# Performance work log

Hardware: AMD Instinct MI355X
Metric: run time of the kernel (lower is better)

Reference implementation:

```python
import jax, jax.numpy as jnp
import numpy as np

B, S, H, D = 16, 1024, 8, 128
HID = 1024
EPS = 1e-5
ALPHA = 1.0 / (D ** 0.5)
SILU_SCALE = 1.0 / S  # silu_scale = 1/max_seq_len


def _layer_norm(x, w, b):
    mu = jnp.mean(x, axis=-1, keepdims=True)
    var = jnp.mean(jnp.square(x - mu), axis=-1, keepdims=True)
    return (x - mu) * jax.lax.rsqrt(var + EPS) * w + b


def setup_inputs() -> dict:
    key = jax.random.key(0)
    ks = jax.random.split(key, 4)
    N = B * S
    return {
        "x": jax.random.normal(ks[0], (N, HID), dtype=jnp.float32),
        "ln_in_w": jnp.ones((HID,), jnp.float32),
        "ln_in_b": jnp.zeros((HID,), jnp.float32),
        "W_uvqk": jax.random.normal(ks[1], (4 * H * D, HID), jnp.float32) * (HID ** -0.5),
        "b_uvqk": jax.random.normal(ks[2], (4 * H * D,), jnp.float32) * 0.1,
        "ln_out_w": jnp.ones((H * D,), jnp.float32),
        "ln_out_b": jnp.zeros((H * D,), jnp.float32),
        "W_proj": jax.random.normal(ks[3], (H * D, HID), jnp.float32) * ((H * D) ** -0.5),
    }


def reference(x, ln_in_w, ln_in_b, W_uvqk, b_uvqk, ln_out_w, ln_out_b, W_proj):
    # x: [N, HID] jagged tokens (rectangular: B seqs of length S)
    normed = _layer_norm(x, ln_in_w, ln_in_b)
    mixed = jax.nn.silu(normed @ W_uvqk.T + b_uvqk)          # [N, 4*H*D]
    u, v, q, k = jnp.split(mixed, 4, axis=-1)
    q = q.reshape(B, S, H, D)
    k = k.reshape(B, S, H, D)
    v = v.reshape(B, S, H, D)
    # HSTU attention: silu(q.k^T * alpha) * silu_scale, causal per sequence
    scores = jnp.einsum("bshd,bthd->bhst", q, k) * ALPHA      # [B,H,S,S]
    w = jax.nn.silu(scores) * SILU_SCALE
    causal = jnp.tril(jnp.ones((S, S), dtype=bool))
    w = jnp.where(causal, w, 0.0)
    attn = jnp.einsum("bhst,bthd->bshd", w, v).reshape(B * S, H * D)
    parallel = u * _layer_norm(attn, ln_out_w, ln_out_b)
    out = parallel @ W_proj + x  # residual
    return out
```

## Files before the change

### kernel.cpp

```cpp
#include <hip/hip_runtime.h>

typedef __bf16 bf16x8 __attribute__((ext_vector_type(8)));
typedef float f32x4 __attribute__((ext_vector_type(4)));
typedef unsigned short u16x4 __attribute__((ext_vector_type(4)));
typedef unsigned short u16x8 __attribute__((ext_vector_type(8)));

#define DEVI __device__ __forceinline__

DEVI unsigned short f2b(float f) {
  union { float f; unsigned u; } v; v.f = f;
  unsigned r = (v.u + 0x7FFFu + ((v.u >> 16) & 1u)) >> 16;
  return (unsigned short)r;
}
DEVI float b2f(unsigned short h) {
  union { unsigned u; float f; } v; v.u = ((unsigned)h) << 16;
  return v.f;
}
DEVI float silu_f(float v) { return v / (1.f + __expf(-v)); }

DEVI void gload_lds16(const void* g, void* l) {
  __builtin_amdgcn_global_load_lds(
      (const __attribute__((address_space(1))) unsigned int*)g,
      (__attribute__((address_space(3))) unsigned int*)l, 16, 0, 0);
}

#define ALPHA 0.08838834764831845f
#define SILU_SCALE 0.0009765625f
#define LN_EPS 1e-5f

__global__ __launch_bounds__(256, 4) void cvt_bf16_kernel(
    const float* __restrict__ src, unsigned short* __restrict__ dst, int n4) {
  int i = blockIdx.x * 256 + threadIdx.x;
  int stride = gridDim.x * 256;
  for (; i < n4; i += stride) {
    f32x4 f = ((const f32x4*)src)[i];
    u16x4 o;
    #pragma unroll
    for (int j = 0; j < 4; ++j) o[j] = f2b(f[j]);
    ((u16x4*)dst)[i] = o;
  }
}

__global__ __launch_bounds__(256, 4) void transpose_wp_kernel(
    const float* __restrict__ Wp, unsigned short* __restrict__ WpT) {
  __shared__ unsigned short lT[64 * 68];
  int tid = threadIdx.x;
  int r0 = blockIdx.y * 64, c0 = blockIdx.x * 64;
  #pragma unroll
  for (int p = 0; p < 4; ++p) {
    int r = p * 16 + (tid >> 4);
    int c = (tid & 15) * 4;
    f32x4 f = *(const f32x4*)(Wp + (size_t)(r0 + r) * 1024 + c0 + c);
    #pragma unroll
    for (int i = 0; i < 4; ++i) lT[(c + i) * 68 + r] = f2b(f[i]);
  }
  __syncthreads();
  #pragma unroll
  for (int p = 0; p < 4; ++p) {
    int j = p * 16 + (tid >> 4);
    int i0 = (tid & 15) * 4;
    u16x4 o;
    #pragma unroll
    for (int q = 0; q < 4; ++q) o[q] = lT[j * 68 + i0 + q];
    *(u16x4*)(WpT + (size_t)(c0 + j) * 1024 + r0 + i0) = o;
  }
}

__global__ __launch_bounds__(256, 4) void ln1_kernel(
    const float* __restrict__ x, const float* __restrict__ w,
    const float* __restrict__ bwt, unsigned short* __restrict__ out) {
  __shared__ float red[8];
  int row = blockIdx.x, tid = threadIdx.x;
  f32x4 f = ((const f32x4*)(x + (size_t)row * 1024))[tid];
  float s1 = f[0] + f[1] + f[2] + f[3];
  float s2 = f[0] * f[0] + f[1] * f[1] + f[2] * f[2] + f[3] * f[3];
  #pragma unroll
  for (int off = 32; off > 0; off >>= 1) {
    s1 += __shfl_down(s1, off);
    s2 += __shfl_down(s2, off);
  }
  if ((tid & 63) == 0) { red[(tid >> 6) * 2] = s1; red[(tid >> 6) * 2 + 1] = s2; }
  __syncthreads();
  s1 = red[0] + red[2] + red[4] + red[6];
  s2 = red[1] + red[3] + red[5] + red[7];
  float mu = s1 * (1.f / 1024.f);
  float rstd = rsqrtf(s2 * (1.f / 1024.f) - mu * mu + LN_EPS);
  f32x4 wv = ((const f32x4*)w)[tid];
  f32x4 bv = ((const f32x4*)bwt)[tid];
  u16x4 o;
  #pragma unroll
  for (int i = 0; i < 4; ++i) o[i] = f2b((f[i] - mu) * rstd * wv[i] + bv[i]);
  ((u16x4*)(out + (size_t)row * 1024))[tid] = o;
}

__global__ __launch_bounds__(256, 4) void ln2_kernel(
    const unsigned short* __restrict__ attn, unsigned short* __restrict__ mixed,
    const float* __restrict__ w, const float* __restrict__ bwt) {
  __shared__ float red[8];
  int row = blockIdx.x, tid = threadIdx.x;
  u16x4 av = ((const u16x4*)(attn + (size_t)row * 1024))[tid];
  float f0 = b2f(av[0]), f1 = b2f(av[1]), f2v = b2f(av[2]), f3 = b2f(av[3]);
  float s1 = f0 + f1 + f2v + f3;
  float s2 = f0 * f0 + f1 * f1 + f2v * f2v + f3 * f3;
  #pragma unroll
  for (int off = 32; off > 0; off >>= 1) {
    s1 += __shfl_down(s1, off);
    s2 += __shfl_down(s2, off);
  }
  if ((tid & 63) == 0) { red[(tid >> 6) * 2] = s1; red[(tid >> 6) * 2 + 1] = s2; }
  __syncthreads();
  s1 = red[0] + red[2] + red[4] + red[6];
  s2 = red[1] + red[3] + red[5] + red[7];
  float mu = s1 * (1.f / 1024.f);
  float rstd = rsqrtf(s2 * (1.f / 1024.f) - mu * mu + LN_EPS);
  f32x4 wv = ((const f32x4*)w)[tid];
  f32x4 bv = ((const f32x4*)bwt)[tid];
  u16x4 uv = ((const u16x4*)(mixed + (size_t)row * 4096))[tid];
  float n0 = (f0 - mu) * rstd * wv[0] + bv[0];
  float n1 = (f1 - mu) * rstd * wv[1] + bv[1];
  float n2 = (f2v - mu) * rstd * wv[2] + bv[2];
  float n3 = (f3 - mu) * rstd * wv[3] + bv[3];
  u16x4 o;
  o[0] = f2b(b2f(uv[0]) * n0);
  o[1] = f2b(b2f(uv[1]) * n1);
  o[2] = f2b(b2f(uv[2]) * n2);
  o[3] = f2b(b2f(uv[3]) * n3);
  ((u16x4*)(mixed + (size_t)row * 4096 + 1024))[tid] = o;
}

template <int EPI>
__global__ __launch_bounds__(256, 2) void gemm_bt_kernel(
    const unsigned short* __restrict__ A, int lda,
    const unsigned short* __restrict__ Bt, int ldb,
    unsigned short* __restrict__ Cb, float* __restrict__ Cf, int ldc,
    const float* __restrict__ aux, int K) {
  __shared__ unsigned short lA[128 * 64];
  __shared__ unsigned short lB[128 * 64];
  const int tid = threadIdx.x, wave = tid >> 6, lane = tid & 63;
  const int row0 = blockIdx.x * 128, col0 = blockIdx.y * 128;
  const int wr = wave >> 1, wc = wave & 1;
  const int sr = tid >> 3;
  const int kel = ((tid & 7) ^ (sr & 7)) * 8;
  f32x4 acc[4][4] = {};
  for (int k0 = 0; k0 < K; k0 += 64) {
    #pragma unroll
    for (int is = 0; is < 4; ++is) {
      int r = is * 32 + sr;
      gload_lds16(A + (size_t)(row0 + r) * lda + k0 + kel, lA + is * 2048 + wave * 512);
      gload_lds16(Bt + (size_t)(col0 + r) * ldb + k0 + kel, lB + is * 2048 + wave * 512);
    }
    __syncthreads();
    #pragma unroll
    for (int kk = 0; kk < 2; ++kk) {
      const int cb = (lane >> 4) * 16 + kk * 64;
      bf16x8 af[4], bfr[4];
      #pragma unroll
      for (int i = 0; i < 4; ++i) {
        int ra = wr * 64 + i * 16 + (lane & 15);
        af[i] = *(const bf16x8*)(lA + ra * 64 + ((cb ^ ((ra & 7) << 4)) >> 1));
        int rb = wc * 64 + i * 16 + (lane & 15);
        bfr[i] = *(const bf16x8*)(lB + rb * 64 + ((cb ^ ((rb & 7) << 4)) >> 1));
      }
      #pragma unroll
      for (int i = 0; i < 4; ++i)
        #pragma unroll
        for (int j = 0; j < 4; ++j)
          acc[i][j] = __builtin_amdgcn_mfma_f32_16x16x32_bf16(af[i], bfr[j], acc[i][j], 0, 0, 0);
    }
    __syncthreads();
  }
  const int cr = (lane >> 4) * 4, cc = lane & 15;
  #pragma unroll
  for (int i = 0; i < 4; ++i) {
    int grow0 = row0 + wr * 64 + i * 16 + cr;
    #pragma unroll
    for (int j = 0; j < 4; ++j) {
      int gcol = col0 + wc * 64 + j * 16 + cc;
      if (EPI == 0) {
        float bvv = aux[gcol];
        #pragma unroll
        for (int r = 0; r < 4; ++r)
          Cb[(size_t)(grow0 + r) * ldc + gcol] = f2b(silu_f(acc[i][j][r] + bvv));
      } else {
        #pragma unroll
        for (int r = 0; r < 4; ++r) {
          size_t idx = (size_t)(grow0 + r) * ldc + gcol;
          Cf[idx] = acc[i][j][r] + aux[idx];
        }
      }
    }
  }
}

__global__ __launch_bounds__(256, 4) void vtrans_kernel(
    const unsigned short* __restrict__ mixed, unsigned short* __restrict__ vT) {
  __shared__ unsigned short lT[128 * 64];
  const int tid = threadIdx.x;
  const int s0 = blockIdx.x * 64, h = blockIdx.y, b = blockIdx.z;
  const unsigned short* vp = mixed + (size_t)b * 1024 * 4096 + 1024 + h * 128;
  #pragma unroll
  for (int p = 0; p < 4; ++p) {
    int sl = p * 16 + (tid >> 4);
    int d0 = (tid & 15) * 8;
    u16x8 val = *(const u16x8*)(vp + (size_t)(s0 + sl) * 4096 + d0);
    #pragma unroll
    for (int i = 0; i < 8; ++i) {
      int d = d0 + i;
      lT[d * 64 + ((((sl * 2) ^ ((((d >> 3) & 7)) << 4))) >> 1)] = val[i];
    }
  }
  __syncthreads();
  unsigned short* op = vT + (size_t)(b * 8 + h) * 128 * 1024;
  #pragma unroll
  for (int p = 0; p < 4; ++p) {
    int d = p * 32 + (tid >> 3);
    int sg = (tid & 7) * 8;
    u16x8 o = *(const u16x8*)(lT + d * 64 + ((((sg * 2) ^ ((((d >> 3) & 7)) << 4))) >> 1));
    *(u16x8*)(op + (size_t)d * 1024 + s0 + sg) = o;
  }
}

__global__ __launch_bounds__(256, 2) void attn_kernel(
    const unsigned short* __restrict__ mixed, const unsigned short* __restrict__ vT,
    unsigned short* __restrict__ attnout) {
  __shared__ unsigned short lK[64 * 128];
  __shared__ unsigned short lV[128 * 64];
  __shared__ unsigned short lW[4 * 16 * 64];
  const int tid = threadIdx.x, wave = tid >> 6, lane = tid & 63;
  const int blkq = blockIdx.x, h = blockIdx.y, b = blockIdx.z;
  const int Q0 = blkq * 64;
  const size_t rowbase = (size_t)b * 1024 * 4096;
  const unsigned short* qp = mixed + rowbase + 2048 + h * 128;
  const unsigned short* kp = mixed + rowbase + 3072 + h * 128;
  const unsigned short* vp = vT + (size_t)(b * 8 + h) * 128 * 1024;
  bf16x8 qf[4];
  {
    int qrow = Q0 + wave * 16 + (lane & 15);
    #pragma unroll
    for (int kk = 0; kk < 4; ++kk)
      qf[kk] = *(const bf16x8*)(qp + (size_t)qrow * 4096 + (lane >> 4) * 8 + kk * 32);
  }
  f32x4 oacc[8] = {};
  unsigned short* lWw = lW + wave * 1024;
  for (int t0 = 0; t0 <= Q0; t0 += 64) {
    {
      int rr = tid >> 4, gg = tid & 15;
      #pragma unroll
      for (int is = 0; is < 4; ++is) {
        int row = is * 16 + rr;
        gload_lds16(kp + (size_t)(t0 + row) * 4096 + (size_t)((gg ^ (row & 7)) * 8),
                    lK + is * 2048 + wave * 512);
      }
      int dr = tid >> 3, g2 = tid & 7;
      #pragma unroll
      for (int is = 0; is < 4; ++is) {
        int d = is * 32 + dr;
        gload_lds16(vp + (size_t)d * 1024 + t0 + ((g2 ^ (d & 7)) * 8),
                    lV + is * 2048 + wave * 512);
      }
    }
    __syncthreads();
    f32x4 sacc[4] = {};
    #pragma unroll
    for (int kk = 0; kk < 4; ++kk) {
      #pragma unroll
      for (int f = 0; f < 4; ++f) {
        int trow = f * 16 + (lane & 15);
        int cb = (lane >> 4) * 16 + kk * 64;
        bf16x8 kf = *(const bf16x8*)(lK + trow * 128 + ((cb ^ ((trow & 7) << 4)) >> 1));
        sacc[f] = __builtin_amdgcn_mfma_f32_16x16x32_bf16(qf[kk], kf, sacc[f], 0, 0, 0);
      }
    }
    const bool diag = (t0 == Q0);
    #pragma unroll
    for (int f = 0; f < 4; ++f) {
      int t = f * 16 + (lane & 15);
      #pragma unroll
      for (int r = 0; r < 4; ++r) {
        int q = (lane >> 4) * 4 + r;
        float s = sacc[f][r] * ALPHA;
        float w = silu_f(s) * SILU_SCALE;
        if (diag && t > wave * 16 + q) w = 0.f;
        lWw[q * 64 + (((t * 2) ^ ((q & 7) << 4)) >> 1)] = f2b(w);
      }
    }
    #pragma unroll
    for (int kk = 0; kk < 2; ++kk) {
      int qr = lane & 15;
      int cb = (lane >> 4) * 16 + kk * 64;
      bf16x8 wf = *(const bf16x8*)(lWw + qr * 64 + ((cb ^ ((qr & 7) << 4)) >> 1));
      #pragma unroll
      for (int nf = 0; nf < 8; ++nf) {
        int dr2 = nf * 16 + (lane & 15);
        bf16x8 vf = *(const bf16x8*)(lV + dr2 * 64 + ((cb ^ ((dr2 & 7) << 4)) >> 1));
        oacc[nf] = __builtin_amdgcn_mfma_f32_16x16x32_bf16(wf, vf, oacc[nf], 0, 0, 0);
      }
    }
    __syncthreads();
  }
  const int cr = (lane >> 4) * 4, cc = lane & 15;
  #pragma unroll
  for (int nf = 0; nf < 8; ++nf) {
    int d = nf * 16 + cc;
    #pragma unroll
    for (int r = 0; r < 4; ++r) {
      int q = Q0 + wave * 16 + cr + r;
      attnout[((size_t)b * 1024 + q) * 1024 + h * 128 + d] = f2b(oacc[nf][r]);
    }
  }
}

extern "C" void kernel_launch(void* const* d_in, const int* in_sizes, int n_in,
                              void* d_out, int out_size, void* d_ws, size_t ws_size,
                              hipStream_t stream) {
  const float* x        = (const float*)d_in[0];
  const float* ln_in_w  = (const float*)d_in[1];
  const float* ln_in_b  = (const float*)d_in[2];
  const float* W_uvqk   = (const float*)d_in[3];
  const float* b_uvqk   = (const float*)d_in[4];
  const float* ln_out_w = (const float*)d_in[5];
  const float* ln_out_b = (const float*)d_in[6];
  const float* W_proj   = (const float*)d_in[7];
  float* out = (float*)d_out;
  char* ws = (char*)d_ws;

  unsigned short* Wq  = (unsigned short*)(ws);
  unsigned short* WpT = (unsigned short*)(ws + 8388608);
  unsigned short* nrm = (unsigned short*)(ws + 10485760);
  unsigned short* mix = (unsigned short*)(ws + 44040192);
  unsigned short* vT  = (unsigned short*)(ws + 178257920);

  cvt_bf16_kernel<<<2048, 256, 0, stream>>>(W_uvqk, Wq, 4194304 / 4);
  transpose_wp_kernel<<<dim3(16, 16), 256, 0, stream>>>(W_proj, WpT);
  ln1_kernel<<<16384, 256, 0, stream>>>(x, ln_in_w, ln_in_b, nrm);
  gemm_bt_kernel<0><<<dim3(128, 32), 256, 0, stream>>>(nrm, 1024, Wq, 1024, mix,
                                                       (float*)nullptr, 4096, b_uvqk, 1024);
  vtrans_kernel<<<dim3(16, 8, 16), 256, 0, stream>>>(mix, vT);
  attn_kernel<<<dim3(16, 8, 16), 256, 0, stream>>>(mix, vT, nrm);
  ln2_kernel<<<16384, 256, 0, stream>>>(nrm, mix, ln_out_w, ln_out_b);
  gemm_bt_kernel<1><<<dim3(128, 8), 256, 0, stream>>>(mix + 1024, 4096, WpT, 1024,
                                                      (unsigned short*)nullptr, out, 1024, x, 1024);
}
```

Measured before the change: 512.7 us.

## Replace GEMM with 256x256-tile, 8-wave, double-buffered pipelined kernel

Replaces the 128x128 single-buffered GEMM with a 256x256 tile kernel using 512 threads. It double-buffers LDS with split K-halves, issues global-to-LDS loads two tiles ahead, interleaves them with MFMA phases, and adds s_setprio and an XCD-aware block swizzle. The goal is to hide global load latency and raise arithmetic intensity per LDS load for both GEMMs. The costs are 128KB of LDS and higher register pressure, which limit occupancy, and the projection GEMM now launches only 256 workgroups.

After: 521.1 us. No clear change (+1.6%).

```diff
diff --git a/kernel.cpp b/kernel.cpp
--- a/kernel.cpp
+++ b/kernel.cpp
@@ -129,50 +129,140 @@
 }
 
 template <int EPI>
-__global__ __launch_bounds__(256, 2) void gemm_bt_kernel(
+__global__ __launch_bounds__(512, 2) void gemm256_kernel(
     const unsigned short* __restrict__ A, int lda,
     const unsigned short* __restrict__ Bt, int ldb,
     unsigned short* __restrict__ Cb, float* __restrict__ Cf, int ldc,
     const float* __restrict__ aux, int K) {
-  __shared__ unsigned short lA[128 * 64];
-  __shared__ unsigned short lB[128 * 64];
+  __shared__ unsigned short lds[65536];
   const int tid = threadIdx.x, wave = tid >> 6, lane = tid & 63;
-  const int row0 = blockIdx.x * 128, col0 = blockIdx.y * 128;
-  const int wr = wave >> 1, wc = wave & 1;
-  const int sr = tid >> 3;
-  const int kel = ((tid & 7) ^ (sr & 7)) * 8;
-  f32x4 acc[4][4] = {};
-  for (int k0 = 0; k0 < K; k0 += 64) {
-    #pragma unroll
-    for (int is = 0; is < 4; ++is) {
-      int r = is * 32 + sr;
-      gload_lds16(A + (size_t)(row0 + r) * lda + k0 + kel, lA + is * 2048 + wave * 512);
-      gload_lds16(Bt + (size_t)(col0 + r) * ldb + k0 + kel, lB + is * 2048 + wave * 512);
-    }
-    __syncthreads();
-    #pragma unroll
-    for (int kk = 0; kk < 2; ++kk) {
-      const int cb = (lane >> 4) * 16 + kk * 64;
-      bf16x8 af[4], bfr[4];
-      #pragma unroll
-      for (int i = 0; i < 4; ++i) {
-        int ra = wr * 64 + i * 16 + (lane & 15);
-        af[i] = *(const bf16x8*)(lA + ra * 64 + ((cb ^ ((ra & 7) << 4)) >> 1));
-        int rb = wc * 64 + i * 16 + (lane & 15);
-        bfr[i] = *(const bf16x8*)(lB + rb * 64 + ((cb ^ ((rb & 7) << 4)) >> 1));
-      }
-      #pragma unroll
-      for (int i = 0; i < 4; ++i)
-        #pragma unroll
-        for (int j = 0; j < 4; ++j)
-          acc[i][j] = __builtin_amdgcn_mfma_f32_16x16x32_bf16(af[i], bfr[j], acc[i][j], 0, 0, 0);
-    }
-    __syncthreads();
-  }
-  const int cr = (lane >> 4) * 4, cc = lane & 15;
-  #pragma unroll
-  for (int i = 0; i < 4; ++i) {
-    int grow0 = row0 + wr * 64 + i * 16 + cr;
+  const int gx = gridDim.x;
+  const int nwg = gx * gridDim.y;
+  const int lin = blockIdx.y * gx + blockIdx.x;
+  const int swz = (lin & 7) * (nwg >> 3) + (lin >> 3);
+  const int row0 = (swz % gx) * 256, col0 = (swz / gx) * 256;
+  const int wr = wave >> 2, wc = wave & 3;
+
+  const unsigned short* Ab = A + (size_t)row0 * lda;
+  const unsigned short* Bb = Bt + (size_t)col0 * ldb;
+
+  const int pl = wave * 64 + lane;
+
+  auto stage = [&](const unsigned short* src, int ld, int lbase, int t, int kh) {
+    unsigned short* dst = lds + lbase + (t & 1) * 16384 + kh * 8192;
+    const unsigned short* s = src + t * 64 + kh * 32;
+    #pragma unroll
+    for (int c = 0; c < 2; ++c) {
+      int p = c * 512 + pl;
+      int row = p >> 2;
+      int g = (p ^ (p >> 2) ^ (p >> 4)) & 3;
+      gload_lds16(s + (size_t)row * ld + g * 8, dst + (c * 512 + wave * 64) * 8);
+    }
+  };
+
+  const int slot = ((lane >> 4) ^ lane ^ (lane >> 2)) & 3;
+  const int aoff = (wr * 128 + (lane & 15)) * 32 + slot * 8;
+  const int boff = (wc * 64 + (lane & 15)) * 32 + slot * 8;
+
+  f32x4 acc[8][4];
+  #pragma unroll
+  for (int i = 0; i < 8; ++i)
+    #pragma unroll
+    for (int j = 0; j < 4; ++j) acc[i][j] = f32x4{0.f, 0.f, 0.f, 0.f};
+
+  stage(Ab, lda, 0, 0, 0);
+  stage(Bb, ldb, 32768, 0, 0);
+  stage(Ab, lda, 0, 0, 1);
+  stage(Bb, ldb, 32768, 0, 1);
+  stage(Ab, lda, 0, 1, 0);
+  stage(Bb, ldb, 32768, 1, 0);
+  stage(Ab, lda, 0, 1, 1);
+  asm volatile("s_waitcnt vmcnt(6)" ::: "memory");
+  __builtin_amdgcn_s_barrier();
+
+  const int NT = K >> 6;
+  for (int t = 0; t < NT; ++t) {
+    const int bo = (t & 1) * 16384;
+    const unsigned short* lA0 = lds + bo;
+    const unsigned short* lA1 = lds + bo + 8192;
+    const unsigned short* lB0 = lds + 32768 + bo;
+    const unsigned short* lB1 = lds + 32768 + bo + 8192;
+    bf16x8 af[8], b0, b1;
+
+    #pragma unroll
+    for (int i = 0; i < 8; ++i) af[i] = *(const bf16x8*)(lA0 + aoff + i * 512);
+    b0 = *(const bf16x8*)(lB0 + boff);
+    b1 = *(const bf16x8*)(lB0 + boff + 512);
+    if (t + 1 < NT) stage(Bb, ldb, 32768, t + 1, 1);
+    __builtin_amdgcn_s_barrier();
+    asm volatile("s_waitcnt lgkmcnt(0)" ::: "memory");
+    __builtin_amdgcn_sched_barrier(0);
+    __builtin_amdgcn_s_setprio(1);
+    #pragma unroll
+    for (int i = 0; i < 8; ++i) {
+      acc[i][0] = __builtin_amdgcn_mfma_f32_16x16x32_bf16(af[i], b0, acc[i][0], 0, 0, 0);
+      acc[i][1] = __builtin_amdgcn_mfma_f32_16x16x32_bf16(af[i], b1, acc[i][1], 0, 0, 0);
+    }
+    __builtin_amdgcn_s_setprio(0);
+    __builtin_amdgcn_s_barrier();
+
+    b0 = *(const bf16x8*)(lB0 + boff + 2 * 512);
+    b1 = *(const bf16x8*)(lB0 + boff + 3 * 512);
+    if (t + 2 < NT) stage(Ab, lda, 0, t + 2, 0);
+    __builtin_amdgcn_s_barrier();
+    asm volatile("s_waitcnt lgkmcnt(0)" ::: "memory");
+    __builtin_amdgcn_sched_barrier(0);
+    __builtin_amdgcn_s_setprio(1);
+    #pragma unroll
+    for (int i = 0; i < 8; ++i) {
+      acc[i][2] = __builtin_amdgcn_mfma_f32_16x16x32_bf16(af[i], b0, acc[i][2], 0, 0, 0);
+      acc[i][3] = __builtin_amdgcn_mfma_f32_16x16x32_bf16(af[i], b1, acc[i][3], 0, 0, 0);
+    }
+    __builtin_amdgcn_s_setprio(0);
+    __builtin_amdgcn_s_barrier();
+
+    #pragma unroll
+    for (int i = 0; i < 8; ++i) af[i] = *(const bf16x8*)(lA1 + aoff + i * 512);
+    b0 = *(const bf16x8*)(lB1 + boff);
+    b1 = *(const bf16x8*)(lB1 + boff + 512);
+    if (t + 2 < NT) stage(Bb, ldb, 32768, t + 2, 0);
+    __builtin_amdgcn_s_barrier();
+    asm volatile("s_waitcnt lgkmcnt(0)" ::: "memory");
+    __builtin_amdgcn_sched_barrier(0);
+    __builtin_amdgcn_s_setprio(1);
+    #pragma unroll
+    for (int i = 0; i < 8; ++i) {
+      acc[i][0] = __builtin_amdgcn_mfma_f32_16x16x32_bf16(af[i], b0, acc[i][0], 0, 0, 0);
+      acc[i][1] = __builtin_amdgcn_mfma_f32_16x16x32_bf16(af[i], b1, acc[i][1], 0, 0, 0);
+    }
+    __builtin_amdgcn_s_setprio(0);
+    __builtin_amdgcn_s_barrier();
+
+    b0 = *(const bf16x8*)(lB1 + boff + 2 * 512);
+    b1 = *(const bf16x8*)(lB1 + boff + 3 * 512);
+    if (t + 2 < NT) stage(Ab, lda, 0, t + 2, 1);
+    __builtin_amdgcn_s_barrier();
+    asm volatile("s_waitcnt lgkmcnt(0)" ::: "memory");
+    __builtin_amdgcn_sched_barrier(0);
+    __builtin_amdgcn_s_setprio(1);
+    #pragma unroll
+    for (int i = 0; i < 8; ++i) {
+      acc[i][2] = __builtin_amdgcn_mfma_f32_16x16x32_bf16(af[i], b0, acc[i][2], 0, 0, 0);
+      acc[i][3] = __builtin_amdgcn_mfma_f32_16x16x32_bf16(af[i], b1, acc[i][3], 0, 0, 0);
+    }
+    __builtin_amdgcn_s_setprio(0);
+    if (t + 2 < NT) {
+      asm volatile("s_waitcnt vmcnt(6)" ::: "memory");
+    } else {
+      asm volatile("s_waitcnt vmcnt(0)" ::: "memory");
+    }
+    __builtin_amdgcn_s_barrier();
+  }
+
+  const int cr4 = (lane >> 4) * 4, cc = lane & 15;
+  #pragma unroll
+  for (int i = 0; i < 8; ++i) {
+    int grow0 = row0 + wr * 128 + i * 16 + cr4;
     #pragma unroll
     for (int j = 0; j < 4; ++j) {
       int gcol = col0 + wc * 64 + j * 16 + cc;
@@ -333,11 +423,11 @@
   cvt_bf16_kernel<<<2048, 256, 0, stream>>>(W_uvqk, Wq, 4194304 / 4);
   transpose_wp_kernel<<<dim3(16, 16), 256, 0, stream>>>(W_proj, WpT);
   ln1_kernel<<<16384, 256, 0, stream>>>(x, ln_in_w, ln_in_b, nrm);
-  gemm_bt_kernel<0><<<dim3(128, 32), 256, 0, stream>>>(nrm, 1024, Wq, 1024, mix,
-                                                       (float*)nullptr, 4096, b_uvqk, 1024);
+  gemm256_kernel<0><<<dim3(64, 16), 512, 0, stream>>>(nrm, 1024, Wq, 1024, mix,
+                                                      (float*)nullptr, 4096, b_uvqk, 1024);
   vtrans_kernel<<<dim3(16, 8, 16), 256, 0, stream>>>(mix, vT);
   attn_kernel<<<dim3(16, 8, 16), 256, 0, stream>>>(mix, vT, nrm);
   ln2_kernel<<<16384, 256, 0, stream>>>(nrm, mix, ln_out_w, ln_out_b);
-  gemm_bt_kernel<1><<<dim3(128, 8), 256, 0, stream>>>(mix + 1024, 4096, WpT, 1024,
-                                                      (unsigned short*)nullptr, out, 1024, x, 1024);
-}
+  gemm256_kernel<1><<<dim3(64, 4), 512, 0, stream>>>(mix + 1024, 4096, WpT, 1024,
+                                                     (unsigned short*)nullptr, out, 1024, x, 1024);
+}
```
